# Performance work log

Hardware: AMD Instinct MI355X
Metric: run time of the kernel (lower is better)

Reference implementation:

```python
import jax, jax.numpy as jnp
import numpy as np

B, T, C, H, DH = 4, 2048, 1024, 16, 64  # batch, seq (block_size), n_embd, heads, head_size


def setup_inputs() -> dict:
    key = jax.random.key(0)
    ks = jax.random.split(key, 6)
    x = jax.random.normal(ks[0], (B, T, C), dtype=jnp.float32)
    init = 0.02
    Wq = jax.random.normal(ks[1], (H, C, DH), dtype=jnp.float32) * init
    Wk = jax.random.normal(ks[2], (H, C, DH), dtype=jnp.float32) * init
    Wv = jax.random.normal(ks[3], (H, C, DH), dtype=jnp.float32) * init
    Wp = jax.random.normal(ks[4], (H * DH, C), dtype=jnp.float32) * init
    bp = jnp.zeros((C,), dtype=jnp.float32)
    return {"x": x, "Wq": Wq, "Wk": Wk, "Wv": Wv, "Wp": Wp, "bp": bp}


def reference(x, Wq, Wk, Wv, Wp, bp):
    Bb, Tt, Cc = x.shape
    # per-head projections, vectorized over heads (original loops in Python)
    q = jnp.einsum('btc,hcd->bhtd', x, Wq)
    k = jnp.einsum('btc,hcd->bhtd', x, Wk)
    v = jnp.einsum('btc,hcd->bhtd', x, Wv)
    # NOTE: original scales by rsqrt(C) where C is the INPUT embed dim, not head_size
    scale = 1.0 / jnp.sqrt(jnp.asarray(Cc, dtype=x.dtype))
    wei = jnp.einsum('bhtd,bhsd->bhts', q, k) * scale  # [B,H,T,T]
    causal = jnp.tril(jnp.ones((Tt, Tt), dtype=bool))
    wei = jnp.where(causal, wei, -jnp.inf)
    wei = jax.nn.softmax(wei, axis=-1)
    out = jnp.einsum('bhts,bhsd->bhtd', wei, v)  # [B,H,T,DH]
    # concat heads along feature axis (head h -> slice h*DH:(h+1)*DH)
    out = out.transpose(0, 2, 1, 3).reshape(Bb, Tt, -1)  # [B,T,H*DH]
    out = out @ Wp + bp  # output projection to n_embd
    return out
```

## Files before the change

### kernel.cpp

```cpp
#include <hip/hip_runtime.h>

#define TSEQ 2048
#define CDIM 1024
#define NH 16
#define DH 64
#define NB 4

typedef __bf16 bf16x8 __attribute__((ext_vector_type(8)));
typedef float f32x4 __attribute__((ext_vector_type(4)));

#define QSCALE 0.04508422f

static __device__ __forceinline__ ushort f2bf(float f) {
  unsigned u = __float_as_uint(f);
  unsigned r = u + 0x7fffu + ((u >> 16) & 1u);
  return (ushort)(r >> 16);
}

static __device__ __forceinline__ uint cvtpk(float lo, float hi) {
  uint r;
  asm("v_cvt_pk_bf16_f32 %0, %1, %2" : "=v"(r) : "v"(lo), "v"(hi));
  return r;
}

static __device__ __forceinline__ void gload_lds16(const void* g, void* ldsbase) {
  __builtin_amdgcn_global_load_lds((const __attribute__((address_space(1))) void*)g,
                                   (__attribute__((address_space(3))) void*)ldsbase,
                                   16, 0, 0);
}

__global__ void cvt_x_kernel(const float4* __restrict__ src, ushort4* __restrict__ dst, int n4) {
  int i = blockIdx.x * blockDim.x + threadIdx.x;
  if (i >= n4) return;
  float4 f = src[i];
  ushort4 o;
  o.x = f2bf(f.x); o.y = f2bf(f.y); o.z = f2bf(f.z); o.w = f2bf(f.w);
  dst[i] = o;
}

__global__ void transpose_cvt_kernel(const float* __restrict__ src, ushort* __restrict__ dst,
                                     int R, int Cc) {
  __shared__ float tile[32][33];
  const float* s = src + (size_t)blockIdx.z * R * Cc;
  ushort* d = dst + (size_t)blockIdx.z * R * Cc;
  int c0 = blockIdx.x * 32, r0 = blockIdx.y * 32;
  int tx = threadIdx.x, ty = threadIdx.y;
  for (int i = ty; i < 32; i += 8) {
    int r = r0 + i, c = c0 + tx;
    tile[i][tx] = (r < R && c < Cc) ? s[(size_t)r * Cc + c] : 0.f;
  }
  __syncthreads();
  for (int i = ty; i < 32; i += 8) {
    int c = c0 + i, r = r0 + tx;
    if (c < Cc && r < R) d[(size_t)c * R + r] = f2bf(tile[tx][i]);
  }
}

template <int MODE>
__global__ __launch_bounds__(256) void gemm_kernel(
    const ushort* __restrict__ A, const ushort* __restrict__ Bt,
    const float* __restrict__ bp, float* __restrict__ fout,
    ushort* __restrict__ qb, ushort* __restrict__ kb, ushort* __restrict__ vTb) {
  __shared__ ushort lds[16384];
  const int tid = threadIdx.x, w = tid >> 6, l = tid & 63;
  const int nwg = gridDim.x;
  const int bid = blockIdx.x;
  const int wgid = (bid & 7) * (nwg >> 3) + (bid >> 3);
  const int mt = wgid & 63, nt = wgid >> 6;
  const int wr = w >> 1, wc = w & 1;
  const int srow = l >> 3;
  const int scol = (((l & 7) ^ srow) << 3);
  char* ldsb = (char*)lds;

  f32x4 acc[4][4] = {};

  for (int k0 = 0; k0 < CDIM; k0 += 64) {
#pragma unroll
    for (int i = 0; i < 8; ++i) {
      int ch = w * 8 + i;
      if (ch < 16) {
        gload_lds16(A + ((size_t)mt * 128 + ch * 8 + srow) * CDIM + k0 + scol, ldsb + ch * 1024);
      } else {
        gload_lds16(Bt + ((size_t)nt * 128 + (ch - 16) * 8 + srow) * CDIM + k0 + scol,
                    ldsb + ch * 1024);
      }
    }
    __syncthreads();
#pragma unroll
    for (int ks = 0; ks < 2; ++ks) {
      bf16x8 af[4];
#pragma unroll
      for (int fm = 0; fm < 4; ++fm) {
        int row = wr * 64 + fm * 16 + (l & 15);
        int cb = (ks * 64 + 16 * (l >> 4)) ^ ((row & 7) << 4);
        af[fm] = *(const bf16x8*)(ldsb + row * 128 + cb);
      }
#pragma unroll
      for (int fn = 0; fn < 4; ++fn) {
        int n = wc * 64 + fn * 16 + (l & 15);
        int cb = (ks * 64 + 16 * (l >> 4)) ^ ((n & 7) << 4);
        bf16x8 bfr = *(const bf16x8*)(ldsb + 16384 + n * 128 + cb);
#pragma unroll
        for (int fm = 0; fm < 4; ++fm)
          acc[fm][fn] = __builtin_amdgcn_mfma_f32_16x16x32_bf16(af[fm], bfr, acc[fm][fn], 0, 0, 0);
      }
    }
    __syncthreads();
  }

#pragma unroll
  for (int fm = 0; fm < 4; ++fm) {
#pragma unroll
    for (int fn = 0; fn < 4; ++fn) {
      const int gr0 = mt * 128 + wr * 64 + fm * 16 + (l >> 4) * 4;
      const int gc = nt * 128 + wc * 64 + fn * 16 + (l & 15);
      if (MODE == 1) {
        float bias = bp[gc];
#pragma unroll
        for (int r = 0; r < 4; ++r)
          fout[(size_t)(gr0 + r) * CDIM + gc] = acc[fm][fn][r] + bias;
      } else {
        const int sel = gc >> 10, h = (gc >> 6) & 15, d = gc & 63;
        const int bh = (gr0 >> 11) * NH + h, tl = gr0 & 2047;
        if (sel == 2) {
          ushort4 pk;
          pk.x = f2bf(acc[fm][fn][0]); pk.y = f2bf(acc[fm][fn][1]);
          pk.z = f2bf(acc[fm][fn][2]); pk.w = f2bf(acc[fm][fn][3]);
          *(ushort4*)(vTb + ((size_t)bh * DH + d) * TSEQ + tl) = pk;
        } else if (sel == 0) {
#pragma unroll
          for (int r = 0; r < 4; ++r)
            qb[((size_t)bh * TSEQ + tl + r) * DH + d] = f2bf(acc[fm][fn][r] * QSCALE);
        } else {
#pragma unroll
          for (int r = 0; r < 4; ++r)
            kb[((size_t)bh * TSEQ + tl + r) * DH + d] = f2bf(acc[fm][fn][r]);
        }
      }
    }
  }
}

__global__ __launch_bounds__(512, 4) void attn_kernel(
    const ushort* __restrict__ qb, const ushort* __restrict__ kb,
    const ushort* __restrict__ vTb, ushort* __restrict__ aob) {
  __shared__ ushort lds[16384];
  char* ldsb = (char*)lds;
  const int tid = threadIdx.x, w = tid >> 6, l = tid & 63;
  const int id = blockIdx.x;
  const int bh = (id & 7) * 8 + ((id >> 3) & 7);
  const int pr = id >> 6;
  const int b = bh >> 4, h = bh & 15;
  const int g = l >> 4, q = l & 15;
  const int srow = l >> 3;
  const int scol = (((l & 7) ^ srow) << 3);
  const int adrA = ((l & 16) << 1 | q) << 2;
  const int adrB = adrA + 64;
  const bool hi32 = (l & 32) != 0;

#pragma unroll 1
  for (int pass = 0; pass < 2; ++pass) {
    const int qt = pass ? (15 - pr) : pr;
    const int q0 = qt * 128;
    const int nt = 2 * (qt + 1);

    bf16x8 qf[2];
    {
      const ushort* qrow = qb + ((size_t)bh * TSEQ + q0 + w * 16 + q) * DH;
      qf[0] = *(const bf16x8*)(qrow + 8 * g);
      qf[1] = *(const bf16x8*)(qrow + 32 + 8 * g);
    }

    float m = -1e30f, lsum = 0.f;
    f32x4 o[4] = {};

#pragma unroll
    for (int i = 0; i < 2; ++i) {
      int ch = w * 2 + i;
      if (ch < 8)
        gload_lds16(kb + ((size_t)bh * TSEQ + ch * 8 + srow) * DH + scol, ldsb + ch * 1024);
      else {
        int d = (ch - 8) * 8 + srow;
        gload_lds16(vTb + ((size_t)bh * DH + d) * TSEQ + scol, ldsb + 16384 + (ch - 8) * 1024);
      }
    }

#pragma unroll 1
    for (int j = 0; j < nt; ++j) {
      __syncthreads();
      const int cbuf = j & 1;
      const int kv0 = j * 64;
      if (j + 1 < nt) {
        const int kvn = (j + 1) * 64, nb = (j + 1) & 1;
#pragma unroll
        for (int i = 0; i < 2; ++i) {
          int ch = w * 2 + i;
          if (ch < 8)
            gload_lds16(kb + ((size_t)bh * TSEQ + kvn + ch * 8 + srow) * DH + scol,
                        ldsb + nb * 8192 + ch * 1024);
          else {
            int d = (ch - 8) * 8 + srow;
            gload_lds16(vTb + ((size_t)bh * DH + d) * TSEQ + kvn + scol,
                        ldsb + 16384 + nb * 8192 + (ch - 8) * 1024);
          }
        }
      }
      char* Kb = ldsb + cbuf * 8192;
      char* Vb = ldsb + 16384 + cbuf * 8192;

      f32x4 s[4] = {};
      __builtin_amdgcn_s_setprio(1);
#pragma unroll
      for (int ks = 0; ks < 2; ++ks)
#pragma unroll
        for (int fn = 0; fn < 4; ++fn) {
          int n = fn * 16 + q;
          int cbb = (ks * 64 + 16 * g) ^ ((n & 7) << 4);
          bf16x8 kf = *(const bf16x8*)(Kb + n * 128 + cbb);
          s[fn] = __builtin_amdgcn_mfma_f32_16x16x32_bf16(kf, qf[ks], s[fn], 0, 0, 0);
        }
      __builtin_amdgcn_s_setprio(0);

      if (j >= nt - 2) {
        int rowloc = q0 + w * 16 + q - kv0;
#pragma unroll
        for (int fn = 0; fn < 4; ++fn)
#pragma unroll
          for (int r = 0; r < 4; ++r)
            if (fn * 16 + 4 * g + r > rowloc) s[fn][r] = -1e30f;
      }

      float rm = fmaxf(fmaxf(fmaxf(s[0][0], s[0][1]), fmaxf(s[0][2], s[0][3])),
                       fmaxf(fmaxf(s[1][0], s[1][1]), fmaxf(s[1][2], s[1][3])));
      rm = fmaxf(rm, fmaxf(fmaxf(fmaxf(s[2][0], s[2][1]), fmaxf(s[2][2], s[2][3])),
                           fmaxf(fmaxf(s[3][0], s[3][1]), fmaxf(s[3][2], s[3][3]))));
      rm = fmaxf(rm, __shfl_xor(rm, 16));
      rm = fmaxf(rm, __shfl_xor(rm, 32));

      if (__any(rm - m > 8.f)) {
        float mn = fmaxf(m, rm);
        float fc = __builtin_amdgcn_exp2f(m - mn);
        m = mn; lsum *= fc;
#pragma unroll
        for (int r = 0; r < 4; ++r) {
          float fcq = __shfl(fc, (l & 0x30) | (4 * g + r), 64);
#pragma unroll
          for (int fn = 0; fn < 4; ++fn) o[fn][r] *= fcq;
        }
      }

      uint D[4][2];
      float rs = 0.f;
#pragma unroll
      for (int fn = 0; fn < 4; ++fn) {
        float p0 = __builtin_amdgcn_exp2f(s[fn][0] - m);
        float p1 = __builtin_amdgcn_exp2f(s[fn][1] - m);
        float p2 = __builtin_amdgcn_exp2f(s[fn][2] - m);
        float p3 = __builtin_amdgcn_exp2f(s[fn][3] - m);
        rs += (p0 + p1) + (p2 + p3);
        D[fn][0] = cvtpk(p0, p1);
        D[fn][1] = cvtpk(p2, p3);
      }
      rs += __shfl_xor(rs, 16);
      rs += __shfl_xor(rs, 32);
      lsum += rs;

#pragma unroll
      for (int ks = 0; ks < 2; ++ks) {
        uint t0a = __builtin_amdgcn_ds_bpermute(adrA, (int)D[2 * ks][0]);
        uint t0b = __builtin_amdgcn_ds_bpermute(adrA, (int)D[2 * ks + 1][0]);
        uint t1a = __builtin_amdgcn_ds_bpermute(adrA, (int)D[2 * ks][1]);
        uint t1b = __builtin_amdgcn_ds_bpermute(adrA, (int)D[2 * ks + 1][1]);
        uint t2a = __builtin_amdgcn_ds_bpermute(adrB, (int)D[2 * ks][0]);
        uint t2b = __builtin_amdgcn_ds_bpermute(adrB, (int)D[2 * ks + 1][0]);
        uint t3a = __builtin_amdgcn_ds_bpermute(adrB, (int)D[2 * ks][1]);
        uint t3b = __builtin_amdgcn_ds_bpermute(adrB, (int)D[2 * ks + 1][1]);
        union { uint u[4]; bf16x8 v; } P;
        P.u[0] = hi32 ? t0b : t0a;
        P.u[1] = hi32 ? t1b : t1a;
        P.u[2] = hi32 ? t2b : t2a;
        P.u[3] = hi32 ? t3b : t3a;
        __builtin_amdgcn_s_setprio(1);
#pragma unroll
        for (int fn = 0; fn < 4; ++fn) {
          int n = fn * 16 + q;
          int cbb = (ks * 64 + 16 * g) ^ ((n & 7) << 4);
          bf16x8 vf = *(const bf16x8*)(Vb + n * 128 + cbb);
          o[fn] = __builtin_amdgcn_mfma_f32_16x16x32_bf16(P.v, vf, o[fn], 0, 0, 0);
        }
        __builtin_amdgcn_s_setprio(0);
      }
    }

    float inv = 1.f / lsum;
#pragma unroll
    for (int r = 0; r < 4; ++r) {
      float invq = __shfl(inv, (l & 0x30) | (4 * g + r), 64);
      int t = q0 + w * 16 + 4 * g + r;
#pragma unroll
      for (int fn = 0; fn < 4; ++fn) {
        int d = fn * 16 + q;
        aob[((size_t)b * TSEQ + t) * (NH * DH) + h * DH + d] = f2bf(o[fn][r] * invq);
      }
    }
    __syncthreads();
  }
}

extern "C" void kernel_launch(void* const* d_in, const int* in_sizes, int n_in,
                              void* d_out, int out_size, void* d_ws, size_t ws_size,
                              hipStream_t stream) {
  (void)in_sizes; (void)n_in; (void)out_size; (void)ws_size;
  const float* x  = (const float*)d_in[0];
  const float* Wq = (const float*)d_in[1];
  const float* Wk = (const float*)d_in[2];
  const float* Wv = (const float*)d_in[3];
  const float* Wp = (const float*)d_in[4];
  const float* bp = (const float*)d_in[5];
  float* out = (float*)d_out;
  char* ws = (char*)d_ws;

  ushort* xb  = (ushort*)(ws);
  ushort* wall = (ushort*)(ws + (16ull << 20));
  ushort* wqT = wall;
  ushort* wkT = wall + (1ull << 20);
  ushort* wvT = wall + (2ull << 20);
  ushort* wpT = (ushort*)(ws + (22ull << 20));
  ushort* qb  = (ushort*)(ws + (24ull << 20));
  ushort* kb  = (ushort*)(ws + (40ull << 20));
  ushort* vTb = (ushort*)(ws + (56ull << 20));
  ushort* aob = (ushort*)(ws + (72ull << 20));

  cvt_x_kernel<<<(NB * TSEQ * CDIM / 4 + 255) / 256, 256, 0, stream>>>(
      (const float4*)x, (ushort4*)xb, NB * TSEQ * CDIM / 4);
  transpose_cvt_kernel<<<dim3(2, 32, 16), dim3(32, 8), 0, stream>>>(Wq, wqT, CDIM, DH);
  transpose_cvt_kernel<<<dim3(2, 32, 16), dim3(32, 8), 0, stream>>>(Wk, wkT, CDIM, DH);
  transpose_cvt_kernel<<<dim3(2, 32, 16), dim3(32, 8), 0, stream>>>(Wv, wvT, CDIM, DH);
  transpose_cvt_kernel<<<dim3(32, 32, 1), dim3(32, 8), 0, stream>>>(Wp, wpT, CDIM, CDIM);

  gemm_kernel<0><<<dim3(64 * 24), 256, 0, stream>>>(xb, wall, nullptr, nullptr, qb, kb, vTb);
  attn_kernel<<<dim3(512), 512, 0, stream>>>(qb, kb, vTb, aob);
  gemm_kernel<1><<<dim3(64 * 8), 256, 0, stream>>>(aob, wpT, bp, out, nullptr, nullptr, nullptr);
}
```

Before: 198.4 us.

## Double attention KV tile to 128 and remap GEMM tile indexing

New measurement: 187.1 us. 5.7% less time.

```diff
diff --git a/kernel.cpp b/kernel.cpp
--- a/kernel.cpp
+++ b/kernel.cpp
@@ -66,7 +66,8 @@
   const int nwg = gridDim.x;
   const int bid = blockIdx.x;
   const int wgid = (bid & 7) * (nwg >> 3) + (bid >> 3);
-  const int mt = wgid & 63, nt = wgid >> 6;
+  const int NT = (MODE == 0) ? 24 : 8;
+  const int nt = wgid % NT, mt = wgid / NT;
   const int wr = w >> 1, wc = w & 1;
   const int srow = l >> 3;
   const int scol = (((l & 7) ^ srow) << 3);
@@ -144,7 +145,7 @@
 __global__ __launch_bounds__(512, 4) void attn_kernel(
     const ushort* __restrict__ qb, const ushort* __restrict__ kb,
     const ushort* __restrict__ vTb, ushort* __restrict__ aob) {
-  __shared__ ushort lds[16384];
+  __shared__ ushort lds[32768];
   char* ldsb = (char*)lds;
   const int tid = threadIdx.x, w = tid >> 6, l = tid & 63;
   const int id = blockIdx.x;
@@ -162,7 +163,7 @@
   for (int pass = 0; pass < 2; ++pass) {
     const int qt = pass ? (15 - pr) : pr;
     const int q0 = qt * 128;
-    const int nt = 2 * (qt + 1);
+    const int nt = qt + 1;
 
     bf16x8 qf[2];
     {
@@ -175,13 +176,14 @@
     f32x4 o[4] = {};
 
 #pragma unroll
-    for (int i = 0; i < 2; ++i) {
-      int ch = w * 2 + i;
-      if (ch < 8)
+    for (int i = 0; i < 4; ++i) {
+      int ch = w * 4 + i;
+      if (ch < 16)
         gload_lds16(kb + ((size_t)bh * TSEQ + ch * 8 + srow) * DH + scol, ldsb + ch * 1024);
       else {
-        int d = (ch - 8) * 8 + srow;
-        gload_lds16(vTb + ((size_t)bh * DH + d) * TSEQ + scol, ldsb + 16384 + (ch - 8) * 1024);
+        int c = ch - 16, vh = c >> 3;
+        gload_lds16(vTb + ((size_t)bh * DH + (c & 7) * 8 + srow) * TSEQ + 64 * vh + scol,
+                    ldsb + 32768 + vh * 8192 + (c & 7) * 1024);
       }
     }
 
@@ -189,31 +191,30 @@
     for (int j = 0; j < nt; ++j) {
       __syncthreads();
       const int cbuf = j & 1;
-      const int kv0 = j * 64;
       if (j + 1 < nt) {
-        const int kvn = (j + 1) * 64, nb = (j + 1) & 1;
-#pragma unroll
-        for (int i = 0; i < 2; ++i) {
-          int ch = w * 2 + i;
-          if (ch < 8)
+        const int kvn = (j + 1) * 128, nb = (j + 1) & 1;
+#pragma unroll
+        for (int i = 0; i < 4; ++i) {
+          int ch = w * 4 + i;
+          if (ch < 16)
             gload_lds16(kb + ((size_t)bh * TSEQ + kvn + ch * 8 + srow) * DH + scol,
-                        ldsb + nb * 8192 + ch * 1024);
+                        ldsb + nb * 16384 + ch * 1024);
           else {
-            int d = (ch - 8) * 8 + srow;
-            gload_lds16(vTb + ((size_t)bh * DH + d) * TSEQ + kvn + scol,
-                        ldsb + 16384 + nb * 8192 + (ch - 8) * 1024);
+            int c = ch - 16, vh = c >> 3;
+            gload_lds16(vTb + ((size_t)bh * DH + (c & 7) * 8 + srow) * TSEQ + kvn + 64 * vh + scol,
+                        ldsb + 32768 + nb * 16384 + vh * 8192 + (c & 7) * 1024);
           }
         }
       }
-      char* Kb = ldsb + cbuf * 8192;
-      char* Vb = ldsb + 16384 + cbuf * 8192;
-
-      f32x4 s[4] = {};
+      char* Kb = ldsb + cbuf * 16384;
+      char* Vb = ldsb + 32768 + cbuf * 16384;
+
+      f32x4 s[8] = {};
       __builtin_amdgcn_s_setprio(1);
 #pragma unroll
       for (int ks = 0; ks < 2; ++ks)
 #pragma unroll
-        for (int fn = 0; fn < 4; ++fn) {
+        for (int fn = 0; fn < 8; ++fn) {
           int n = fn * 16 + q;
           int cbb = (ks * 64 + 16 * g) ^ ((n & 7) << 4);
           bf16x8 kf = *(const bf16x8*)(Kb + n * 128 + cbb);
@@ -221,19 +222,19 @@
         }
       __builtin_amdgcn_s_setprio(0);
 
-      if (j >= nt - 2) {
-        int rowloc = q0 + w * 16 + q - kv0;
-#pragma unroll
-        for (int fn = 0; fn < 4; ++fn)
+      if (j == nt - 1) {
+        int rowloc = w * 16 + q;
+#pragma unroll
+        for (int fn = 0; fn < 8; ++fn)
 #pragma unroll
           for (int r = 0; r < 4; ++r)
             if (fn * 16 + 4 * g + r > rowloc) s[fn][r] = -1e30f;
       }
 
-      float rm = fmaxf(fmaxf(fmaxf(s[0][0], s[0][1]), fmaxf(s[0][2], s[0][3])),
-                       fmaxf(fmaxf(s[1][0], s[1][1]), fmaxf(s[1][2], s[1][3])));
-      rm = fmaxf(rm, fmaxf(fmaxf(fmaxf(s[2][0], s[2][1]), fmaxf(s[2][2], s[2][3])),
-                           fmaxf(fmaxf(s[3][0], s[3][1]), fmaxf(s[3][2], s[3][3]))));
+      float rm = -1e30f;
+#pragma unroll
+      for (int fn = 0; fn < 8; ++fn)
+        rm = fmaxf(rm, fmaxf(fmaxf(s[fn][0], s[fn][1]), fmaxf(s[fn][2], s[fn][3])));
       rm = fmaxf(rm, __shfl_xor(rm, 16));
       rm = fmaxf(rm, __shfl_xor(rm, 32));
 
@@ -249,10 +250,10 @@
         }
       }
 
-      uint D[4][2];
+      uint D[8][2];
       float rs = 0.f;
 #pragma unroll
-      for (int fn = 0; fn < 4; ++fn) {
+      for (int fn = 0; fn < 8; ++fn) {
         float p0 = __builtin_amdgcn_exp2f(s[fn][0] - m);
         float p1 = __builtin_amdgcn_exp2f(s[fn][1] - m);
         float p2 = __builtin_amdgcn_exp2f(s[fn][2] - m);
@@ -266,26 +267,27 @@
       lsum += rs;
 
 #pragma unroll
-      for (int ks = 0; ks < 2; ++ks) {
-        uint t0a = __builtin_amdgcn_ds_bpermute(adrA, (int)D[2 * ks][0]);
-        uint t0b = __builtin_amdgcn_ds_bpermute(adrA, (int)D[2 * ks + 1][0]);
-        uint t1a = __builtin_amdgcn_ds_bpermute(adrA, (int)D[2 * ks][1]);
-        uint t1b = __builtin_amdgcn_ds_bpermute(adrA, (int)D[2 * ks + 1][1]);
-        uint t2a = __builtin_amdgcn_ds_bpermute(adrB, (int)D[2 * ks][0]);
-        uint t2b = __builtin_amdgcn_ds_bpermute(adrB, (int)D[2 * ks + 1][0]);
-        uint t3a = __builtin_amdgcn_ds_bpermute(adrB, (int)D[2 * ks][1]);
-        uint t3b = __builtin_amdgcn_ds_bpermute(adrB, (int)D[2 * ks + 1][1]);
+      for (int ksg = 0; ksg < 4; ++ksg) {
+        uint t0a = __builtin_amdgcn_ds_bpermute(adrA, (int)D[2 * ksg][0]);
+        uint t0b = __builtin_amdgcn_ds_bpermute(adrA, (int)D[2 * ksg + 1][0]);
+        uint t1a = __builtin_amdgcn_ds_bpermute(adrA, (int)D[2 * ksg][1]);
+        uint t1b = __builtin_amdgcn_ds_bpermute(adrA, (int)D[2 * ksg + 1][1]);
+        uint t2a = __builtin_amdgcn_ds_bpermute(adrB, (int)D[2 * ksg][0]);
+        uint t2b = __builtin_amdgcn_ds_bpermute(adrB, (int)D[2 * ksg + 1][0]);
+        uint t3a = __builtin_amdgcn_ds_bpermute(adrB, (int)D[2 * ksg][1]);
+        uint t3b = __builtin_amdgcn_ds_bpermute(adrB, (int)D[2 * ksg + 1][1]);
         union { uint u[4]; bf16x8 v; } P;
         P.u[0] = hi32 ? t0b : t0a;
         P.u[1] = hi32 ? t1b : t1a;
         P.u[2] = hi32 ? t2b : t2a;
         P.u[3] = hi32 ? t3b : t3a;
+        const int vh = ksg >> 1, ksl = ksg & 1;
         __builtin_amdgcn_s_setprio(1);
 #pragma unroll
         for (int fn = 0; fn < 4; ++fn) {
           int n = fn * 16 + q;
-          int cbb = (ks * 64 + 16 * g) ^ ((n & 7) << 4);
-          bf16x8 vf = *(const bf16x8*)(Vb + n * 128 + cbb);
+          int cbb = (ksl * 64 + 16 * g) ^ ((n & 7) << 4);
+          bf16x8 vf = *(const bf16x8*)(Vb + vh * 8192 + n * 128 + cbb);
           o[fn] = __builtin_amdgcn_mfma_f32_16x16x32_bf16(P.v, vf, o[fn], 0, 0, 0);
         }
         __builtin_amdgcn_s_setprio(0);
```

## Restructure attention to four waves with two query subtiles each, one tile per block

Applied to the files above, without the earlier changes.

New measurement: 185.0 us. -6.8%, faster.

```diff
diff --git a/kernel.cpp b/kernel.cpp
--- a/kernel.cpp
+++ b/kernel.cpp
@@ -66,7 +66,8 @@
   const int nwg = gridDim.x;
   const int bid = blockIdx.x;
   const int wgid = (bid & 7) * (nwg >> 3) + (bid >> 3);
-  const int mt = wgid & 63, nt = wgid >> 6;
+  const int NT = (MODE == 0) ? 24 : 8;
+  const int nt = wgid % NT, mt = wgid / NT;
   const int wr = w >> 1, wc = w & 1;
   const int srow = l >> 3;
   const int scol = (((l & 7) ^ srow) << 3);
@@ -141,7 +142,7 @@
   }
 }
 
-__global__ __launch_bounds__(512, 4) void attn_kernel(
+__global__ __launch_bounds__(256, 3) void attn_kernel(
     const ushort* __restrict__ qb, const ushort* __restrict__ kb,
     const ushort* __restrict__ vTb, ushort* __restrict__ aob) {
   __shared__ ushort lds[16384];
@@ -149,7 +150,9 @@
   const int tid = threadIdx.x, w = tid >> 6, l = tid & 63;
   const int id = blockIdx.x;
   const int bh = (id & 7) * 8 + ((id >> 3) & 7);
-  const int pr = id >> 6;
+  const int qt = 15 - (id >> 6);
+  const int q0 = qt * 128;
+  const int nt = 2 * (qt + 1);
   const int b = bh >> 4, h = bh & 15;
   const int g = l >> 4, q = l & 15;
   const int srow = l >> 3;
@@ -158,152 +161,168 @@
   const int adrB = adrA + 64;
   const bool hi32 = (l & 32) != 0;
 
+  bf16x8 qf[2][2];
+#pragma unroll
+  for (int qs = 0; qs < 2; ++qs) {
+    const ushort* qrow = qb + ((size_t)bh * TSEQ + q0 + w * 32 + qs * 16 + q) * DH;
+    qf[qs][0] = *(const bf16x8*)(qrow + 8 * g);
+    qf[qs][1] = *(const bf16x8*)(qrow + 32 + 8 * g);
+  }
+
+  float m[2] = {-1e30f, -1e30f}, lsum[2] = {0.f, 0.f};
+  f32x4 o[4][2] = {};
+
+#pragma unroll
+  for (int i = 0; i < 4; ++i) {
+    int ch = w * 4 + i;
+    if (ch < 8)
+      gload_lds16(kb + ((size_t)bh * TSEQ + ch * 8 + srow) * DH + scol, ldsb + ch * 1024);
+    else {
+      int d = (ch - 8) * 8 + srow;
+      gload_lds16(vTb + ((size_t)bh * DH + d) * TSEQ + scol, ldsb + 16384 + (ch - 8) * 1024);
+    }
+  }
+
 #pragma unroll 1
-  for (int pass = 0; pass < 2; ++pass) {
-    const int qt = pass ? (15 - pr) : pr;
-    const int q0 = qt * 128;
-    const int nt = 2 * (qt + 1);
-
-    bf16x8 qf[2];
-    {
-      const ushort* qrow = qb + ((size_t)bh * TSEQ + q0 + w * 16 + q) * DH;
-      qf[0] = *(const bf16x8*)(qrow + 8 * g);
-      qf[1] = *(const bf16x8*)(qrow + 32 + 8 * g);
-    }
-
-    float m = -1e30f, lsum = 0.f;
-    f32x4 o[4] = {};
-
-#pragma unroll
-    for (int i = 0; i < 2; ++i) {
-      int ch = w * 2 + i;
-      if (ch < 8)
-        gload_lds16(kb + ((size_t)bh * TSEQ + ch * 8 + srow) * DH + scol, ldsb + ch * 1024);
-      else {
-        int d = (ch - 8) * 8 + srow;
-        gload_lds16(vTb + ((size_t)bh * DH + d) * TSEQ + scol, ldsb + 16384 + (ch - 8) * 1024);
-      }
-    }
-
-#pragma unroll 1
-    for (int j = 0; j < nt; ++j) {
-      __syncthreads();
-      const int cbuf = j & 1;
-      const int kv0 = j * 64;
-      if (j + 1 < nt) {
-        const int kvn = (j + 1) * 64, nb = (j + 1) & 1;
-#pragma unroll
-        for (int i = 0; i < 2; ++i) {
-          int ch = w * 2 + i;
-          if (ch < 8)
-            gload_lds16(kb + ((size_t)bh * TSEQ + kvn + ch * 8 + srow) * DH + scol,
-                        ldsb + nb * 8192 + ch * 1024);
-          else {
-            int d = (ch - 8) * 8 + srow;
-            gload_lds16(vTb + ((size_t)bh * DH + d) * TSEQ + kvn + scol,
-                        ldsb + 16384 + nb * 8192 + (ch - 8) * 1024);
-          }
+  for (int j = 0; j < nt; ++j) {
+    __syncthreads();
+    const int cbuf = j & 1;
+    if (j + 1 < nt) {
+      const int kvn = (j + 1) * 64, nb = (j + 1) & 1;
+#pragma unroll
+      for (int i = 0; i < 4; ++i) {
+        int ch = w * 4 + i;
+        if (ch < 8)
+          gload_lds16(kb + ((size_t)bh * TSEQ + kvn + ch * 8 + srow) * DH + scol,
+                      ldsb + nb * 8192 + ch * 1024);
+        else {
+          int d = (ch - 8) * 8 + srow;
+          gload_lds16(vTb + ((size_t)bh * DH + d) * TSEQ + kvn + scol,
+                      ldsb + 16384 + nb * 8192 + (ch - 8) * 1024);
         }
       }
-      char* Kb = ldsb + cbuf * 8192;
-      char* Vb = ldsb + 16384 + cbuf * 8192;
-
-      f32x4 s[4] = {};
-      __builtin_amdgcn_s_setprio(1);
-#pragma unroll
-      for (int ks = 0; ks < 2; ++ks)
-#pragma unroll
-        for (int fn = 0; fn < 4; ++fn) {
-          int n = fn * 16 + q;
-          int cbb = (ks * 64 + 16 * g) ^ ((n & 7) << 4);
-          bf16x8 kf = *(const bf16x8*)(Kb + n * 128 + cbb);
-          s[fn] = __builtin_amdgcn_mfma_f32_16x16x32_bf16(kf, qf[ks], s[fn], 0, 0, 0);
-        }
-      __builtin_amdgcn_s_setprio(0);
-
-      if (j >= nt - 2) {
-        int rowloc = q0 + w * 16 + q - kv0;
+    }
+    char* Kb = ldsb + cbuf * 8192;
+    char* Vb = ldsb + 16384 + cbuf * 8192;
+
+    f32x4 s[4][2] = {};
+    __builtin_amdgcn_s_setprio(1);
+#pragma unroll
+    for (int ks = 0; ks < 2; ++ks)
+#pragma unroll
+      for (int fn = 0; fn < 4; ++fn) {
+        int n = fn * 16 + q;
+        int cbb = (ks * 64 + 16 * g) ^ ((n & 7) << 4);
+        bf16x8 kf = *(const bf16x8*)(Kb + n * 128 + cbb);
+        s[fn][0] = __builtin_amdgcn_mfma_f32_16x16x32_bf16(kf, qf[0][ks], s[fn][0], 0, 0, 0);
+        s[fn][1] = __builtin_amdgcn_mfma_f32_16x16x32_bf16(kf, qf[1][ks], s[fn][1], 0, 0, 0);
+      }
+    __builtin_amdgcn_s_setprio(0);
+
+    if (j >= nt - 2) {
+#pragma unroll
+      for (int qs = 0; qs < 2; ++qs) {
+        int rowloc = q0 + w * 32 + qs * 16 + q - j * 64;
 #pragma unroll
         for (int fn = 0; fn < 4; ++fn)
 #pragma unroll
           for (int r = 0; r < 4; ++r)
-            if (fn * 16 + 4 * g + r > rowloc) s[fn][r] = -1e30f;
-      }
-
-      float rm = fmaxf(fmaxf(fmaxf(s[0][0], s[0][1]), fmaxf(s[0][2], s[0][3])),
-                       fmaxf(fmaxf(s[1][0], s[1][1]), fmaxf(s[1][2], s[1][3])));
-      rm = fmaxf(rm, fmaxf(fmaxf(fmaxf(s[2][0], s[2][1]), fmaxf(s[2][2], s[2][3])),
-                           fmaxf(fmaxf(s[3][0], s[3][1]), fmaxf(s[3][2], s[3][3]))));
-      rm = fmaxf(rm, __shfl_xor(rm, 16));
-      rm = fmaxf(rm, __shfl_xor(rm, 32));
-
-      if (__any(rm - m > 8.f)) {
-        float mn = fmaxf(m, rm);
-        float fc = __builtin_amdgcn_exp2f(m - mn);
-        m = mn; lsum *= fc;
-#pragma unroll
-        for (int r = 0; r < 4; ++r) {
-          float fcq = __shfl(fc, (l & 0x30) | (4 * g + r), 64);
-#pragma unroll
-          for (int fn = 0; fn < 4; ++fn) o[fn][r] *= fcq;
-        }
-      }
-
-      uint D[4][2];
+            if (fn * 16 + 4 * g + r > rowloc) s[fn][qs][r] = -1e30f;
+      }
+    }
+
+    float rm[2];
+#pragma unroll
+    for (int qs = 0; qs < 2; ++qs) {
+      float v = -1e30f;
+#pragma unroll
+      for (int fn = 0; fn < 4; ++fn)
+        v = fmaxf(v, fmaxf(fmaxf(s[fn][qs][0], s[fn][qs][1]), fmaxf(s[fn][qs][2], s[fn][qs][3])));
+      v = fmaxf(v, __shfl_xor(v, 16));
+      v = fmaxf(v, __shfl_xor(v, 32));
+      rm[qs] = v;
+    }
+
+    if (__any(fmaxf(rm[0] - m[0], rm[1] - m[1]) > 8.f)) {
+      float fc[2];
+#pragma unroll
+      for (int qs = 0; qs < 2; ++qs) {
+        float mn = fmaxf(m[qs], rm[qs]);
+        fc[qs] = __builtin_amdgcn_exp2f(m[qs] - mn);
+        m[qs] = mn; lsum[qs] *= fc[qs];
+      }
+#pragma unroll
+      for (int r = 0; r < 4; ++r) {
+        float f0 = __shfl(fc[0], (l & 0x30) | (4 * g + r), 64);
+        float f1 = __shfl(fc[1], (l & 0x30) | (4 * g + r), 64);
+#pragma unroll
+        for (int fn = 0; fn < 4; ++fn) { o[fn][0][r] *= f0; o[fn][1][r] *= f1; }
+      }
+    }
+
+    uint D[2][4][2];
+#pragma unroll
+    for (int qs = 0; qs < 2; ++qs) {
       float rs = 0.f;
 #pragma unroll
       for (int fn = 0; fn < 4; ++fn) {
-        float p0 = __builtin_amdgcn_exp2f(s[fn][0] - m);
-        float p1 = __builtin_amdgcn_exp2f(s[fn][1] - m);
-        float p2 = __builtin_amdgcn_exp2f(s[fn][2] - m);
-        float p3 = __builtin_amdgcn_exp2f(s[fn][3] - m);
+        float p0 = __builtin_amdgcn_exp2f(s[fn][qs][0] - m[qs]);
+        float p1 = __builtin_amdgcn_exp2f(s[fn][qs][1] - m[qs]);
+        float p2 = __builtin_amdgcn_exp2f(s[fn][qs][2] - m[qs]);
+        float p3 = __builtin_amdgcn_exp2f(s[fn][qs][3] - m[qs]);
         rs += (p0 + p1) + (p2 + p3);
-        D[fn][0] = cvtpk(p0, p1);
-        D[fn][1] = cvtpk(p2, p3);
+        D[qs][fn][0] = cvtpk(p0, p1);
+        D[qs][fn][1] = cvtpk(p2, p3);
       }
       rs += __shfl_xor(rs, 16);
       rs += __shfl_xor(rs, 32);
-      lsum += rs;
-
-#pragma unroll
-      for (int ks = 0; ks < 2; ++ks) {
-        uint t0a = __builtin_amdgcn_ds_bpermute(adrA, (int)D[2 * ks][0]);
-        uint t0b = __builtin_amdgcn_ds_bpermute(adrA, (int)D[2 * ks + 1][0]);
-        uint t1a = __builtin_amdgcn_ds_bpermute(adrA, (int)D[2 * ks][1]);
-        uint t1b = __builtin_amdgcn_ds_bpermute(adrA, (int)D[2 * ks + 1][1]);
-        uint t2a = __builtin_amdgcn_ds_bpermute(adrB, (int)D[2 * ks][0]);
-        uint t2b = __builtin_amdgcn_ds_bpermute(adrB, (int)D[2 * ks + 1][0]);
-        uint t3a = __builtin_amdgcn_ds_bpermute(adrB, (int)D[2 * ks][1]);
-        uint t3b = __builtin_amdgcn_ds_bpermute(adrB, (int)D[2 * ks + 1][1]);
-        union { uint u[4]; bf16x8 v; } P;
-        P.u[0] = hi32 ? t0b : t0a;
-        P.u[1] = hi32 ? t1b : t1a;
-        P.u[2] = hi32 ? t2b : t2a;
-        P.u[3] = hi32 ? t3b : t3a;
-        __builtin_amdgcn_s_setprio(1);
-#pragma unroll
-        for (int fn = 0; fn < 4; ++fn) {
-          int n = fn * 16 + q;
-          int cbb = (ks * 64 + 16 * g) ^ ((n & 7) << 4);
-          bf16x8 vf = *(const bf16x8*)(Vb + n * 128 + cbb);
-          o[fn] = __builtin_amdgcn_mfma_f32_16x16x32_bf16(P.v, vf, o[fn], 0, 0, 0);
-        }
-        __builtin_amdgcn_s_setprio(0);
-      }
-    }
-
-    float inv = 1.f / lsum;
+      lsum[qs] += rs;
+    }
+
+#pragma unroll
+    for (int ksg = 0; ksg < 2; ++ksg) {
+      union { uint u[4]; bf16x8 v; } P[2];
+#pragma unroll
+      for (int qs = 0; qs < 2; ++qs) {
+        uint t0a = __builtin_amdgcn_ds_bpermute(adrA, (int)D[qs][2 * ksg][0]);
+        uint t0b = __builtin_amdgcn_ds_bpermute(adrA, (int)D[qs][2 * ksg + 1][0]);
+        uint t1a = __builtin_amdgcn_ds_bpermute(adrA, (int)D[qs][2 * ksg][1]);
+        uint t1b = __builtin_amdgcn_ds_bpermute(adrA, (int)D[qs][2 * ksg + 1][1]);
+        uint t2a = __builtin_amdgcn_ds_bpermute(adrB, (int)D[qs][2 * ksg][0]);
+        uint t2b = __builtin_amdgcn_ds_bpermute(adrB, (int)D[qs][2 * ksg + 1][0]);
+        uint t3a = __builtin_amdgcn_ds_bpermute(adrB, (int)D[qs][2 * ksg][1]);
+        uint t3b = __builtin_amdgcn_ds_bpermute(adrB, (int)D[qs][2 * ksg + 1][1]);
+        P[qs].u[0] = hi32 ? t0b : t0a;
+        P[qs].u[1] = hi32 ? t1b : t1a;
+        P[qs].u[2] = hi32 ? t2b : t2a;
+        P[qs].u[3] = hi32 ? t3b : t3a;
+      }
+      __builtin_amdgcn_s_setprio(1);
+#pragma unroll
+      for (int fn = 0; fn < 4; ++fn) {
+        int n = fn * 16 + q;
+        int cbb = (ksg * 64 + 16 * g) ^ ((n & 7) << 4);
+        bf16x8 vf = *(const bf16x8*)(Vb + n * 128 + cbb);
+        o[fn][0] = __builtin_amdgcn_mfma_f32_16x16x32_bf16(P[0].v, vf, o[fn][0], 0, 0, 0);
+        o[fn][1] = __builtin_amdgcn_mfma_f32_16x16x32_bf16(P[1].v, vf, o[fn][1], 0, 0, 0);
+      }
+      __builtin_amdgcn_s_setprio(0);
+    }
+  }
+
+#pragma unroll
+  for (int qs = 0; qs < 2; ++qs) {
+    float inv = 1.f / lsum[qs];
 #pragma unroll
     for (int r = 0; r < 4; ++r) {
       float invq = __shfl(inv, (l & 0x30) | (4 * g + r), 64);
-      int t = q0 + w * 16 + 4 * g + r;
+      int t = q0 + w * 32 + qs * 16 + 4 * g + r;
 #pragma unroll
       for (int fn = 0; fn < 4; ++fn) {
         int d = fn * 16 + q;
-        aob[((size_t)b * TSEQ + t) * (NH * DH) + h * DH + d] = f2bf(o[fn][r] * invq);
-      }
-    }
-    __syncthreads();
+        aob[((size_t)b * TSEQ + t) * (NH * DH) + h * DH + d] = f2bf(o[fn][qs][r] * invq);
+      }
+    }
   }
 }
 
@@ -339,6 +358,6 @@
   transpose_cvt_kernel<<<dim3(32, 32, 1), dim3(32, 8), 0, stream>>>(Wp, wpT, CDIM, CDIM);
 
   gemm_kernel<0><<<dim3(64 * 24), 256, 0, stream>>>(xb, wall, nullptr, nullptr, qb, kb, vTb);
-  attn_kernel<<<dim3(512), 512, 0, stream>>>(qb, kb, vTb, aob);
+  attn_kernel<<<dim3(1024), 256, 0, stream>>>(qb, kb, vTb, aob);
   gemm_kernel<1><<<dim3(64 * 8), 256, 0, stream>>>(aob, wpT, bp, out, nullptr, nullptr, nullptr);
 }
```
